# Kernel optimization log

Hardware: AMD Instinct MI355X
Metric: run time of the kernel (lower is better)

Reference implementation:

```python
import jax, jax.numpy as jnp
from jax import lax
import numpy as np

L, B, D = 2048, 8, 1024
LN_EPS = 1e-5


def setup_inputs() -> dict:
    key = jax.random.key(0)
    k1, k2 = jax.random.split(key)
    x = jax.random.normal(k1, (L, B, D), dtype=jnp.float32)
    c0 = jnp.zeros((B, D), dtype=jnp.float32)
    # nn.Linear(D, 3D, bias=False): weight shape (3D, D), y = x @ W.T
    W = jax.random.normal(k2, (3 * D, D), dtype=jnp.float32) * (1.0 / np.sqrt(D))
    ln_w = jnp.ones((D,), dtype=jnp.float32)
    ln_b = jnp.zeros((D,), dtype=jnp.float32)
    return {"x": x, "c0": c0, "W": W, "ln_w": ln_w, "ln_b": ln_b}


def reference(x, c0, W, ln_w, ln_b):
    # ufr = x @ W.T : (L,B,3D)
    ufr = jnp.einsum('lbd,ed->lbe', x, W)
    u, f, r = jnp.split(ufr, 3, axis=-1)
    f = jax.nn.sigmoid(f)
    r = jax.nn.sigmoid(r)

    # sequential SRU recurrence: c_t = f_t * c_{t-1} + (1 - f_t) * u_t
    def step(c, fu):
        f_t, u_t = fu
        c = f_t * c + (1.0 - f_t) * u_t
        return c, c

    last_c, c_stack = lax.scan(step, c0, (f, u))  # c_stack: (L,B,D)

    hs = r * jnp.tanh(c_stack) + (1.0 - r) * x
    g = jax.nn.gelu(hs, approximate=False)  # torch F.gelu default = exact erf

    mu = jnp.mean(g, axis=-1, keepdims=True)
    var = jnp.mean(jnp.square(g - mu), axis=-1, keepdims=True)
    out = (g - mu) * lax.rsqrt(var + LN_EPS) * ln_w + ln_b
    return (out, last_c)
```

## Files before the change

### kernel.cpp

```cpp
#include <hip/hip_runtime.h>

typedef unsigned short u16;
typedef unsigned int   u32;
typedef __attribute__((ext_vector_type(8))) __bf16 bf16x8;
typedef __attribute__((ext_vector_type(4))) float  f32x4;

#define L_SEQ  2048
#define BATCH  8
#define DIM    1024
#define ROWS   16384
#define N3     3072
#define NCHUNK 64
#define LCHUNK 32
#define NCHAIN 8192

__device__ __forceinline__ float b2f(u16 h) {
  return __builtin_bit_cast(float, (u32)h << 16);
}
__device__ __forceinline__ u32 pk2(float a, float b) {
  u32 r;
  asm("v_cvt_pk_bf16_f32 %0, %1, %2" : "=v"(r) : "v"(a), "v"(b));
  return r;
}
__device__ __forceinline__ u16 f2b(float f) {
  u32 u = __builtin_bit_cast(u32, f);
  return (u16)((u + 0x7fffu + ((u >> 16) & 1u)) >> 16);
}
__device__ __forceinline__ f32x4 mf(bf16x8 a, bf16x8 b, f32x4 c) {
  return __builtin_amdgcn_mfma_f32_16x16x32_bf16(a, b, c, 0, 0, 0);
}

__global__ void k_pack(const float* __restrict__ x, const float* __restrict__ W,
                       u16* __restrict__ apk, u16* __restrict__ wpk) {
  const int NA = 128 * 32 * 8 * 64;
  const int NB = 12 * 32 * 16 * 64;
  int i = blockIdx.x * 256 + threadIdx.x;
  const int stride = gridDim.x * 256;
  for (; i < NA + NB; i += stride) {
    const float* src; u16* dst;
    if (i < NA) {
      int lane = i & 63, fg = (i >> 6) & 7, t = (i >> 9) & 31, mt = i >> 14;
      int row = mt * 128 + fg * 16 + (lane & 15);
      int k   = t * 32 + (lane >> 4) * 8;
      src = x + (size_t)row * DIM + k;
      dst = apk + (size_t)i * 8;
    } else {
      int j = i - NA;
      int lane = j & 63, c = (j >> 6) & 15, t = (j >> 10) & 31, nt = j >> 15;
      int col = nt * 256 + c * 16 + (lane & 15);
      int k   = t * 32 + (lane >> 4) * 8;
      src = W + (size_t)col * DIM + k;
      dst = wpk + (size_t)j * 8;
    }
    float4 v0 = *(const float4*)src;
    float4 v1 = *(const float4*)(src + 4);
    uint4 o;
    o.x = pk2(v0.x, v0.y); o.y = pk2(v0.z, v0.w);
    o.z = pk2(v1.x, v1.y); o.w = pk2(v1.z, v1.w);
    *(uint4*)dst = o;
  }
}

__device__ __forceinline__ void gl_lds16(const u16* g, u16* l) {
  __builtin_amdgcn_global_load_lds((const __attribute__((address_space(1))) void*)g,
                                   (__attribute__((address_space(3))) void*)l,
                                   16, 0, 0);
}

__global__ __launch_bounds__(512, 4) void k_gemm_v4(const u16* __restrict__ apk,
                                                    const u16* __restrict__ wpk,
                                                    u16* __restrict__ C) {
  __shared__ u16 lds[12288];
  const int tid  = threadIdx.x;
  const int lane = tid & 63;
  const int wid  = tid >> 6;
  const int wm = wid >> 2, wn = wid & 3;
  const int lr = lane & 15, lk = lane >> 4;

  const int bid = blockIdx.x;
  const int xcd = bid & 7;
  const int r   = bid >> 3;
  const int byl = r / 12;
  const int bx  = r - byl * 12;
  const int by  = xcd * 16 + byl;

  const u16* srcA = apk + ((((size_t)by * 32) * 8 + wid) * 64 + lane) * 8;
  const u16* srcB = wpk + ((((size_t)bx * 32) * 16 + wn * 4) * 64 + lane) * 8;

  u16* d0 = &lds[wid * 512 + lane * 8];
  u16* d1 = d0 + 4096;
  u16* d2 = d0 + 8192;
  const u16* ldsA = &lds[wm * 2048 + lane * 8];

  f32x4 acc[4][4] = {};
  bf16x8 A0, A1, A2, A3, B0, B1, B2, B3;

  {
    const u16* gb = srcB;
    A0 = *(const bf16x8*)(gb);
    A1 = *(const bf16x8*)(gb + 512);
    A2 = *(const bf16x8*)(gb + 1024);
    A3 = *(const bf16x8*)(gb + 1536);
  }
  __builtin_amdgcn_sched_barrier(0);
  gl_lds16(srcA, d0);
  gl_lds16(srcA + 4096, d1);
  asm volatile("s_waitcnt vmcnt(1)" ::: "memory");
  asm volatile("s_barrier" ::: "memory");

#define GBODY(T, RB, DN, U0,U1,U2,U3, L0,L1,L2,L3, LOADB, STAGEA, WMODE) {   \
    if (LOADB) {                                                             \
      const u16* gb_ = srcB + (size_t)((T) + 1) * 8192;                      \
      L0 = *(const bf16x8*)(gb_);                                            \
      L1 = *(const bf16x8*)(gb_ + 512);                                      \
      L2 = *(const bf16x8*)(gb_ + 1024);                                     \
      L3 = *(const bf16x8*)(gb_ + 1536);                                     \
    }                                                                        \
    __builtin_amdgcn_sched_barrier(0);                                       \
    if (STAGEA) gl_lds16(srcA + (size_t)((T) + 2) * 4096, DN);               \
    const u16* rb_ = ldsA + (RB) * 4096;                                     \
    bf16x8 av0 = *(const bf16x8*)(rb_);                                      \
    bf16x8 av1 = *(const bf16x8*)(rb_ + 512);                                \
    bf16x8 av2 = *(const bf16x8*)(rb_ + 1024);                               \
    bf16x8 av3 = *(const bf16x8*)(rb_ + 1536);                               \
    __builtin_amdgcn_s_setprio(1);                                           \
    acc[0][0]=mf(av0,U0,acc[0][0]); acc[0][1]=mf(av0,U1,acc[0][1]);          \
    acc[0][2]=mf(av0,U2,acc[0][2]); acc[0][3]=mf(av0,U3,acc[0][3]);          \
    acc[1][0]=mf(av1,U0,acc[1][0]); acc[1][1]=mf(av1,U1,acc[1][1]);          \
    acc[1][2]=mf(av1,U2,acc[1][2]); acc[1][3]=mf(av1,U3,acc[1][3]);          \
    acc[2][0]=mf(av2,U0,acc[2][0]); acc[2][1]=mf(av2,U1,acc[2][1]);          \
    acc[2][2]=mf(av2,U2,acc[2][2]); acc[2][3]=mf(av2,U3,acc[2][3]);          \
    acc[3][0]=mf(av3,U0,acc[3][0]); acc[3][1]=mf(av3,U1,acc[3][1]);          \
    acc[3][2]=mf(av3,U2,acc[3][2]); acc[3][3]=mf(av3,U3,acc[3][3]);          \
    __builtin_amdgcn_s_setprio(0);                                           \
    if ((WMODE) == 0)      asm volatile("s_waitcnt vmcnt(1)" ::: "memory");  \
    else if ((WMODE) == 1) asm volatile("s_waitcnt vmcnt(0)" ::: "memory");  \
    if ((WMODE) != 2)      asm volatile("s_barrier" ::: "memory");           \
  }

  for (int t6 = 0; t6 < 30; t6 += 6) {
    GBODY(t6 + 0, 0, d2, A0,A1,A2,A3, B0,B1,B2,B3, 1, 1, 0)
    GBODY(t6 + 1, 1, d0, B0,B1,B2,B3, A0,A1,A2,A3, 1, 1, 0)
    GBODY(t6 + 2, 2, d1, A0,A1,A2,A3, B0,B1,B2,B3, 1, 1, 0)
    GBODY(t6 + 3, 0, d2, B0,B1,B2,B3, A0,A1,A2,A3, 1, 1, 0)
    GBODY(t6 + 4, 1, d0, A0,A1,A2,A3, B0,B1,B2,B3, 1, 1, 0)
    GBODY(t6 + 5, 2, d1, B0,B1,B2,B3, A0,A1,A2,A3, 1, 1, 0)
  }
  GBODY(30, 0, d2, A0,A1,A2,A3, B0,B1,B2,B3, 1, 0, 1)
  GBODY(31, 1, d0, B0,B1,B2,B3, A0,A1,A2,A3, 0, 0, 2)
#undef GBODY

  const bool act = (bx >= 4);
#pragma unroll
  for (int m = 0; m < 4; ++m) {
    const int row0 = by * 128 + wm * 64 + m * 16 + lk * 4;
#pragma unroll
    for (int n = 0; n < 4; ++n) {
      const int col = bx * 256 + wn * 64 + n * 16 + lr;
#pragma unroll
      for (int j = 0; j < 4; ++j) {
        float v = acc[m][n][j];
        if (act) v = 1.f / (1.f + __expf(-v));
        C[(size_t)(row0 + j) * N3 + col] = f2b(v);
      }
    }
  }
}

__global__ __launch_bounds__(256) void k_gemm_reg(const float* __restrict__ A,
                                                  const float* __restrict__ B,
                                                  u16* __restrict__ C) {
  __shared__ u16 lds[8192];
  const int tid  = threadIdx.x;
  const int lane = tid & 63;
  const int wid  = tid >> 6;
  const int wm = wid >> 1, wn = wid & 1;
  const int lr = lane & 15, lk = lane >> 4;
  const int mBase = blockIdx.y << 7;
  const int nBase = blockIdx.x << 7;

  f32x4 acc[4][4] = {};
  const int aoff = (wm * 64 + lr) * 32 + lk * 8;
  const int boff = 4096 + (wn * 64 + lr) * 32 + lk * 8;

  for (int k0 = 0; k0 < DIM; k0 += 32) {
#pragma unroll
    for (int q = 0; q < 4; ++q) {
      const int i  = q * 256 + tid;
      const int rr = i >> 3;
      const int cc = (i & 7) << 2;
      float4 va = *(const float4*)(A + (size_t)(mBase + rr) * DIM + k0 + cc);
      float4 vb = *(const float4*)(B + (size_t)(nBase + rr) * DIM + k0 + cc);
      uint2 pa; pa.x = pk2(va.x, va.y); pa.y = pk2(va.z, va.w);
      uint2 pb; pb.x = pk2(vb.x, vb.y); pb.y = pk2(vb.z, vb.w);
      *(uint2*)&lds[rr * 32 + cc] = pa;
      *(uint2*)&lds[4096 + rr * 32 + cc] = pb;
    }
    __syncthreads();
    bf16x8 av[4], bv[4];
#pragma unroll
    for (int m = 0; m < 4; ++m) av[m] = *(const bf16x8*)&lds[aoff + m * 512];
#pragma unroll
    for (int n = 0; n < 4; ++n) bv[n] = *(const bf16x8*)&lds[boff + n * 512];
#pragma unroll
    for (int m = 0; m < 4; ++m)
#pragma unroll
      for (int n = 0; n < 4; ++n)
        acc[m][n] = mf(av[m], bv[n], acc[m][n]);
    __syncthreads();
  }

  const bool act = (nBase >= DIM);
#pragma unroll
  for (int m = 0; m < 4; ++m) {
    const int row0 = mBase + wm * 64 + m * 16 + lk * 4;
#pragma unroll
    for (int n = 0; n < 4; ++n) {
      const int col = nBase + wn * 64 + n * 16 + lr;
#pragma unroll
      for (int j = 0; j < 4; ++j) {
        float v = acc[m][n][j];
        if (act) v = 1.f / (1.f + __expf(-v));
        C[(size_t)(row0 + j) * N3 + col] = f2b(v);
      }
    }
  }
}

__global__ void k_scanA(const u16* __restrict__ ufr, float* __restrict__ P,
                        float* __restrict__ V) {
  int g = blockIdx.x * 256 + threadIdx.x;
  int j = g >> 13;
  int chain = g & (NCHAIN - 1);
  int b = chain >> 10;
  int d = chain & (DIM - 1);
  const u16* p = ufr + (size_t)((j * LCHUNK) * BATCH + b) * N3 + d;
  float prod = 1.f, v = 0.f;
  for (int t = 0; t < LCHUNK; ++t) {
    float u = b2f(p[0]);
    float f = b2f(p[DIM]);
    v = f * v + (1.f - f) * u;
    prod *= f;
    p += BATCH * N3;
  }
  P[g] = prod; V[g] = v;
}

__global__ void k_scanB(const float* __restrict__ c0, const float* __restrict__ P,
                        const float* __restrict__ V, float* __restrict__ S,
                        float* __restrict__ lastc) {
  int chain = blockIdx.x * 256 + threadIdx.x;
  float c = c0[chain];
  for (int j = 0; j < NCHUNK; ++j) {
    S[j * NCHAIN + chain] = c;
    c = P[j * NCHAIN + chain] * c + V[j * NCHAIN + chain];
  }
  lastc[chain] = c;
}

__global__ __launch_bounds__(1024) void k_scanln(const u16* __restrict__ ufr,
                                                 const float* __restrict__ S,
                                                 const float* __restrict__ x,
                                                 const float* __restrict__ lnw,
                                                 const float* __restrict__ lnb,
                                                 float* __restrict__ out) {
  const int j = blockIdx.x >> 3;
  const int b = blockIdx.x & 7;
  const int d = threadIdx.x;
  const int lane = d & 63, wid = d >> 6;

  float c = S[j * NCHAIN + b * DIM + d];
  const float wgt = lnw[d];
  const float bia = lnb[d];

  const u16*   pu = ufr + (size_t)((j * LCHUNK) * BATCH + b) * N3 + d;
  const float* px = x   + (size_t)((j * LCHUNK) * BATCH + b) * DIM + d;
  float*       po = out + (size_t)((j * LCHUNK) * BATCH + b) * DIM + d;

  __shared__ float red1[16], red2[16];

  u16 cu = pu[0], cf = pu[DIM], cr = pu[2 * DIM];
  float cx = *px;

  for (int t = 0; t < LCHUNK; ++t) {
    const int adv = (t < LCHUNK - 1) ? 1 : 0;
    u16 nu = pu[(size_t)adv * BATCH * N3];
    u16 nf = pu[(size_t)adv * BATCH * N3 + DIM];
    u16 nr = pu[(size_t)adv * BATCH * N3 + 2 * DIM];
    float nx = px[(size_t)adv * BATCH * DIM];

    float u = b2f(cu), f = b2f(cf), rr = b2f(cr), xx = cx;
    c = f * c + (1.f - f) * u;
    float hs = rr * tanhf(c) + (1.f - rr) * xx;
    float g  = 0.5f * hs * (1.f + erff(hs * 0.70710678118654752f));

    float s1 = g, s2 = g * g;
#pragma unroll
    for (int off = 32; off > 0; off >>= 1) {
      s1 += __shfl_down(s1, off, 64);
      s2 += __shfl_down(s2, off, 64);
    }
    if (lane == 0) { red1[wid] = s1; red2[wid] = s2; }
    __syncthreads();
    float S1 = 0.f, S2 = 0.f;
#pragma unroll
    for (int w = 0; w < 16; ++w) { S1 += red1[w]; S2 += red2[w]; }
    float mu  = S1 * (1.f / DIM);
    float var = S2 * (1.f / DIM) - mu * mu;
    float inv = rsqrtf(var + 1e-5f);
    *po = (g - mu) * inv * wgt + bia;
    __syncthreads();

    cu = nu; cf = nf; cr = nr; cx = nx;
    pu += BATCH * N3;
    px += BATCH * DIM;
    po += BATCH * DIM;
  }
}

extern "C" void kernel_launch(void* const* d_in, const int* in_sizes, int n_in,
                              void* d_out, int out_size, void* d_ws, size_t ws_size,
                              hipStream_t stream) {
  (void)in_sizes; (void)n_in; (void)out_size;
  const float* x   = (const float*)d_in[0];
  const float* c0  = (const float*)d_in[1];
  const float* W   = (const float*)d_in[2];
  const float* lnw = (const float*)d_in[3];
  const float* lnb = (const float*)d_in[4];
  float* out   = (float*)d_out;
  float* lastc = out + (size_t)ROWS * DIM;

  char* ws = (char*)d_ws;

  u16* ufr; float *P, *V, *S;
  const size_t FULL_NEED = 140509184;
  if (ws_size >= FULL_NEED) {
    u16* apk = (u16*)ws;
    u16* wpk = (u16*)(ws + 33554432);
    ufr = (u16*)(ws + 39845888);
    P   = (float*)ws;
    V   = (float*)(ws + 2097152);
    S   = (float*)(ws + 4194304);
    k_pack<<<2048, 256, 0, stream>>>(x, W, apk, wpk);
    k_gemm_v4<<<1536, 512, 0, stream>>>(apk, wpk, ufr);
  } else {
    ufr = (u16*)ws;
    P   = (float*)(ws + 100663296);
    V   = (float*)(ws + 102760448);
    S   = (float*)(ws + 104857600);
    dim3 g1(N3 / 128, ROWS / 128);
    k_gemm_reg<<<g1, 256, 0, stream>>>(x, W, ufr);
  }

  k_scanA<<<(NCHUNK * NCHAIN) / 256, 256, 0, stream>>>(ufr, P, V);
  k_scanB<<<NCHAIN / 256, 256, 0, stream>>>(c0, P, V, S, lastc);
  k_scanln<<<NCHUNK * BATCH, 1024, 0, stream>>>(ufr, S, x, lnw, lnb, out);
}
```

Before: 229.2 us.

## Deepen B-operand register prefetch to two stages and reorder block mapping

```diff
diff --git a/kernel.cpp b/kernel.cpp
--- a/kernel.cpp
+++ b/kernel.cpp
@@ -67,7 +67,7 @@
                                    16, 0, 0);
 }
 
-__global__ __launch_bounds__(512, 4) void k_gemm_v4(const u16* __restrict__ apk,
+__global__ __launch_bounds__(512, 4) void k_gemm_v5(const u16* __restrict__ apk,
                                                     const u16* __restrict__ wpk,
                                                     u16* __restrict__ C) {
   __shared__ u16 lds[12288];
@@ -80,8 +80,8 @@
   const int bid = blockIdx.x;
   const int xcd = bid & 7;
   const int r   = bid >> 3;
-  const int byl = r / 12;
-  const int bx  = r - byl * 12;
+  const int byl = r & 15;
+  const int bx  = r >> 4;
   const int by  = xcd * 16 + byl;
 
   const u16* srcA = apk + ((((size_t)by * 32) * 8 + wid) * 64 + lane) * 8;
@@ -93,14 +93,15 @@
   const u16* ldsA = &lds[wm * 2048 + lane * 8];
 
   f32x4 acc[4][4] = {};
-  bf16x8 A0, A1, A2, A3, B0, B1, B2, B3;
+  bf16x8 S00,S01,S02,S03, S10,S11,S12,S13, S20,S21,S22,S23;
 
   {
-    const u16* gb = srcB;
-    A0 = *(const bf16x8*)(gb);
-    A1 = *(const bf16x8*)(gb + 512);
-    A2 = *(const bf16x8*)(gb + 1024);
-    A3 = *(const bf16x8*)(gb + 1536);
+    const u16* gb0 = srcB;
+    S00 = *(const bf16x8*)(gb0);       S01 = *(const bf16x8*)(gb0 + 512);
+    S02 = *(const bf16x8*)(gb0 + 1024); S03 = *(const bf16x8*)(gb0 + 1536);
+    const u16* gb1 = srcB + 8192;
+    S10 = *(const bf16x8*)(gb1);       S11 = *(const bf16x8*)(gb1 + 512);
+    S12 = *(const bf16x8*)(gb1 + 1024); S13 = *(const bf16x8*)(gb1 + 1536);
   }
   __builtin_amdgcn_sched_barrier(0);
   gl_lds16(srcA, d0);
@@ -110,7 +111,7 @@
 
 #define GBODY(T, RB, DN, U0,U1,U2,U3, L0,L1,L2,L3, LOADB, STAGEA, WMODE) {   \
     if (LOADB) {                                                             \
-      const u16* gb_ = srcB + (size_t)((T) + 1) * 8192;                      \
+      const u16* gb_ = srcB + (size_t)((T) + 2) * 8192;                      \
       L0 = *(const bf16x8*)(gb_);                                            \
       L1 = *(const bf16x8*)(gb_ + 512);                                      \
       L2 = *(const bf16x8*)(gb_ + 1024);                                     \
@@ -133,21 +134,18 @@
     acc[3][0]=mf(av3,U0,acc[3][0]); acc[3][1]=mf(av3,U1,acc[3][1]);          \
     acc[3][2]=mf(av3,U2,acc[3][2]); acc[3][3]=mf(av3,U3,acc[3][3]);          \
     __builtin_amdgcn_s_setprio(0);                                           \
-    if ((WMODE) == 0)      asm volatile("s_waitcnt vmcnt(1)" ::: "memory");  \
+    if ((WMODE) == 0)      asm volatile("s_waitcnt vmcnt(5)" ::: "memory");  \
     else if ((WMODE) == 1) asm volatile("s_waitcnt vmcnt(0)" ::: "memory");  \
     if ((WMODE) != 2)      asm volatile("s_barrier" ::: "memory");           \
   }
 
-  for (int t6 = 0; t6 < 30; t6 += 6) {
-    GBODY(t6 + 0, 0, d2, A0,A1,A2,A3, B0,B1,B2,B3, 1, 1, 0)
-    GBODY(t6 + 1, 1, d0, B0,B1,B2,B3, A0,A1,A2,A3, 1, 1, 0)
-    GBODY(t6 + 2, 2, d1, A0,A1,A2,A3, B0,B1,B2,B3, 1, 1, 0)
-    GBODY(t6 + 3, 0, d2, B0,B1,B2,B3, A0,A1,A2,A3, 1, 1, 0)
-    GBODY(t6 + 4, 1, d0, A0,A1,A2,A3, B0,B1,B2,B3, 1, 1, 0)
-    GBODY(t6 + 5, 2, d1, B0,B1,B2,B3, A0,A1,A2,A3, 1, 1, 0)
-  }
-  GBODY(30, 0, d2, A0,A1,A2,A3, B0,B1,B2,B3, 1, 0, 1)
-  GBODY(31, 1, d0, B0,B1,B2,B3, A0,A1,A2,A3, 0, 0, 2)
+  for (int t3 = 0; t3 < 30; t3 += 3) {
+    GBODY(t3 + 0, 0, d2, S00,S01,S02,S03, S20,S21,S22,S23, 1, 1, 0)
+    GBODY(t3 + 1, 1, d0, S10,S11,S12,S13, S00,S01,S02,S03, 1, 1, 0)
+    GBODY(t3 + 2, 2, d1, S20,S21,S22,S23, S10,S11,S12,S13, 1, 1, 0)
+  }
+  GBODY(30, 0, d2, S00,S01,S02,S03, S20,S21,S22,S23, 0, 0, 1)
+  GBODY(31, 1, d0, S10,S11,S12,S13, S00,S01,S02,S03, 0, 0, 2)
 #undef GBODY
 
   const bool act = (bx >= 4);
@@ -342,7 +340,7 @@
     V   = (float*)(ws + 2097152);
     S   = (float*)(ws + 4194304);
     k_pack<<<2048, 256, 0, stream>>>(x, W, apk, wpk);
-    k_gemm_v4<<<1536, 512, 0, stream>>>(apk, wpk, ufr);
+    k_gemm_v5<<<1536, 512, 0, stream>>>(apk, wpk, ufr);
   } else {
     ufr = (u16*)ws;
     P   = (float*)(ws + 100663296);
```

Result: slower. 391.5 us (+70.8%).
